# Performance work log

Measured on AMD Instinct MI355X. Metric: run time of the kernel, lower is better.

The kernel has to match this reference:

```python
import jax, jax.numpy as jnp
import numpy as np

H = 4  # num_heads


def _ln(x, g, b, eps=1e-5):
    m = x.mean(-1, keepdims=True)
    v = ((x - m) ** 2).mean(-1, keepdims=True)
    return (x - m) / jnp.sqrt(v + eps) * g + b


def setup_inputs() -> dict:
    key = jax.random.key(0)
    ks = jax.random.split(key, 16)
    B, N, M, dQ, dK, dV = 4, 2048, 2048, 128, 128, 128
    s = 0.02
    return {
        "Q": jax.random.normal(ks[0], (B, N, dQ), jnp.float32),
        "K": jax.random.normal(ks[1], (B, M, dK), jnp.float32),
        "adj_mask": jax.random.randint(ks[2], (B, N, M), 0, 2, jnp.int32),
        "Wq": jax.random.normal(ks[3], (dQ, dV), jnp.float32) * s,
        "bq": jnp.zeros((dV,), jnp.float32),
        "Wk": jax.random.normal(ks[4], (dK, dV), jnp.float32) * s,
        "bk": jnp.zeros((dV,), jnp.float32),
        "Wv": jax.random.normal(ks[5], (dK, dV), jnp.float32) * s,
        "bv": jnp.zeros((dV,), jnp.float32),
        "Wr1": jax.random.normal(ks[6], (dV, dV), jnp.float32) * s,
        "br1": jnp.zeros((dV,), jnp.float32),
        "Wr2": jax.random.normal(ks[7], (dV, dV), jnp.float32) * s,
        "br2": jnp.zeros((dV,), jnp.float32),
        "g0": jnp.ones((dV,), jnp.float32),
        "be0": jnp.zeros((dV,), jnp.float32),
        "g1": jnp.ones((dV,), jnp.float32),
        "be1": jnp.zeros((dV,), jnp.float32),
    }


def reference(Q, K, adj_mask, Wq, bq, Wk, bk, Wv, bv, Wr1, br1, Wr2, br2, g0, be0, g1, be1):
    B, N, _ = Q.shape
    M = K.shape[1]
    dV = Wq.shape[1]
    dh = dV // H
    Qp = Q @ Wq + bq   # [B,N,dV]
    Kp = K @ Wk + bk   # [B,M,dV]
    Vp = K @ Wv + bv   # [B,M,dV]
    # torch: split dim_V into H chunks, cat along dim 0 -> head-major [H*B, L, dh]
    def to_heads(x, L):
        return x.reshape(B, L, H, dh).transpose(2, 0, 1, 3).reshape(H * B, L, dh)
    Qh, Kh, Vh = to_heads(Qp, N), to_heads(Kp, M), to_heads(Vp, M)
    attn = jnp.einsum('bnd,bmd->bnm', Qh, Kh) / jnp.sqrt(jnp.float32(dh))  # [H*B,N,M]
    # torch repeat_interleave(mask, H, dim=0) gives batch-major order -- faithful
    mask = jnp.repeat(adj_mask, H, axis=0)
    attn = jnp.where(mask == 0, -jnp.inf, attn)
    A = jax.nn.softmax(attn, axis=2)
    O = Qh + jnp.einsum('bnm,bmd->bnd', A, Vh)  # [H*B,N,dh]
    # recombine heads back to [B,N,dV] (intended split(dim=0)/cat(dim=2))
    O = O.reshape(H, B, N, dh).transpose(1, 2, 0, 3).reshape(B, N, dV)
    O = _ln(O, g0, be0)
    O = O + (jax.nn.relu(O @ Wr1 + br1) @ Wr2 + br2)
    return _ln(O, g1, be1)
```

## Files before the change

### kernel.cpp

```cpp
#include <hip/hip_runtime.h>
#include <hip/hip_bf16.h>


typedef short bf16x8 __attribute__((ext_vector_type(8)));
typedef float f32x4 __attribute__((ext_vector_type(4)));

#define BN 4
#define SEQ 2048
#define DIM 128
#define NH 4
#define DH 32
#define ROWS (BN * SEQ)
#define MS 4
#define MWORDS (SEQ / 32)

static __device__ __forceinline__ unsigned short f2bf(float f) {
    __hip_bfloat16 h = __float2bfloat16(f);
    return *reinterpret_cast<unsigned short*>(&h);
}
static __device__ __forceinline__ float bf2f(unsigned short u) {
    union { unsigned int i; float f; } cv;
    cv.i = ((unsigned int)u) << 16;
    return cv.f;
}
static __device__ __forceinline__ unsigned int pack2bf(float a, float b) {
    return (unsigned int)f2bf(a) | ((unsigned int)f2bf(b) << 16);
}

__global__ __launch_bounds__(256) void pack_prep(
    const int* __restrict__ adj,
    const float* __restrict__ Wq, const float* __restrict__ Wk,
    const float* __restrict__ Wv, const float* __restrict__ W1,
    const float* __restrict__ W2,
    unsigned int* __restrict__ bits, unsigned short* __restrict__ WT)
{
    const int bx = blockIdx.x;
    const int t = threadIdx.x;
    if (bx >= 1024) {
        const float* Ws[5] = {Wq, Wk, Wv, W1, W2};
        const float* W = Ws[bx - 1024];
        unsigned short* out = WT + (bx - 1024) * DIM * DIM;
        for (int i = t; i < DIM * DIM; i += 256) {
            int n = i >> 7, k = i & 127;
            out[i] = f2bf(W[k * DIM + n]);
        }
        return;
    }
    __shared__ unsigned int sB[8][65];
    const int q0 = bx * 8;
#pragma unroll
    for (int i = 0; i < 2; ++i) {
        int widl = i * 256 + t;
        int ql = widl >> 6, wd = widl & 63;
        const int4* src = (const int4*)(adj + (long)(q0 + ql) * SEQ + wd * 32);
        unsigned int w = 0;
#pragma unroll
        for (int j = 0; j < 8; ++j) {
            int4 v = src[j];
            w |= (((unsigned)v.x & 1u) << (4 * j))
               | (((unsigned)v.y & 1u) << (4 * j + 1))
               | (((unsigned)v.z & 1u) << (4 * j + 2))
               | (((unsigned)v.w & 1u) << (4 * j + 3));
        }
        sB[ql][wd] = w;
    }
    __syncthreads();
    const int h = q0 >> 11, qh0 = q0 & 2047;
#pragma unroll
    for (int i = 0; i < 2; ++i) {
        int idx = i * 256 + t;
        int wd = idx >> 3, ql = idx & 7;
        bits[((long)h * MWORDS + wd) * SEQ + qh0 + ql] = sB[ql][wd];
    }
}

__global__ __launch_bounds__(256) void proj_kernel(
    const float* __restrict__ Q, const float* __restrict__ K,
    const float* __restrict__ bq, const float* __restrict__ bk,
    const float* __restrict__ bv, const unsigned short* __restrict__ WT,
    float* __restrict__ Qp, unsigned short* __restrict__ Qb,
    unsigned short* __restrict__ Kb, unsigned short* __restrict__ Vt)
{
    __shared__ __align__(16) unsigned short sX[32][136];
    __shared__ __align__(16) unsigned short sY[32][137];

    const int proj = blockIdx.y;
    const int rowbase = blockIdx.x * 32;
    const float* X = (proj == 0) ? Q : K;
    const unsigned short* Wt = WT + proj * DIM * DIM;
    const float* bias = (proj == 0) ? bq : (proj == 1) ? bk : bv;
    const int bidx = rowbase >> 11;
    const int srowbase = rowbase & 2047;

    const int t = threadIdx.x;
#pragma unroll
    for (int i = 0; i < 4; ++i) {
        int idx = i * 256 + t;
        int row = idx >> 5, c4 = (idx & 31) * 4;
        float4 v = *(const float4*)(X + (long)(rowbase + row) * DIM + c4);
        sX[row][c4 + 0] = f2bf(v.x);
        sX[row][c4 + 1] = f2bf(v.y);
        sX[row][c4 + 2] = f2bf(v.z);
        sX[row][c4 + 3] = f2bf(v.w);
    }
    __syncthreads();

    const int w = t >> 6, lane = t & 63;
    const int n16 = lane & 15, quad = lane >> 4;

    f32x4 acc[2][2];
#pragma unroll
    for (int r = 0; r < 2; ++r)
#pragma unroll
        for (int ct = 0; ct < 2; ++ct)
            acc[r][ct] = (f32x4){0.f, 0.f, 0.f, 0.f};

    for (int ks = 0; ks < 4; ++ks) {
        bf16x8 bfrag[2];
#pragma unroll
        for (int ct = 0; ct < 2; ++ct) {
            int ncol = w * 32 + ct * 16 + n16;
            bfrag[ct] = *(const bf16x8*)(Wt + ncol * DIM + ks * 32 + quad * 8);
        }
#pragma unroll
        for (int r = 0; r < 2; ++r) {
            bf16x8 afrag = *(const bf16x8*)(&sX[r * 16 + n16][ks * 32 + quad * 8]);
#pragma unroll
            for (int ct = 0; ct < 2; ++ct)
                acc[r][ct] = __builtin_amdgcn_mfma_f32_16x16x32_bf16(
                    afrag, bfrag[ct], acc[r][ct], 0, 0, 0);
        }
    }

#pragma unroll
    for (int r = 0; r < 2; ++r) {
#pragma unroll
        for (int ct = 0; ct < 2; ++ct) {
            int col = w * 32 + ct * 16 + n16;
            int hh = col >> 5, dd = col & 31;
            float bv_ = bias[col];
#pragma unroll
            for (int i = 0; i < 4; ++i) {
                int lrow = r * 16 + quad * 4 + i;
                int grow = rowbase + lrow;
                int srow = srowbase + lrow;
                float val = acc[r][ct][i] + bv_;
                if (proj == 0) {
                    Qp[(long)grow * DIM + col] = val;
                    Qb[((long)(hh * BN + bidx) * SEQ + srow) * DH + dd]
                        = f2bf(val * 0.17677669529663687f);
                } else if (proj == 1) {
                    Kb[((long)(hh * BN + bidx) * SEQ + srow) * DH + dd] = f2bf(val);
                } else {
                    sY[lrow][col] = f2bf(val);
                }
            }
        }
    }
    if (proj == 2) {
        __syncthreads();
#pragma unroll
        for (int i = 0; i < 16; ++i) {
            int idx = i * 256 + t;
            int c = idx >> 5, m = idx & 31;
            Vt[((long)bidx * DIM + c) * SEQ + srowbase + m] = sY[m][c];
        }
    }
}

__global__ __launch_bounds__(256, 2) void attn_kernel(
    const unsigned short* __restrict__ Qb, const unsigned short* __restrict__ Kb,
    const unsigned short* __restrict__ Vt, const unsigned int* __restrict__ mbits,
    unsigned short* __restrict__ Opart, float* __restrict__ Lpart)
{
    __shared__ __align__(16) unsigned short sP[4][32][68];

    const int id = blockIdx.x;
    const int combo = id & 15;
    const int qidx = id >> 4;
    const int h = combo >> 2;
    const int sp = combo & 3;
    const int qbase = qidx * 32;
    const int t = threadIdx.x;
    const int b = t >> 6;
    const int lane = t & 63, n16 = lane & 15, quad = lane >> 4;

    const unsigned short* Qh = Qb + ((long)(h * BN + b) * SEQ) * DH + quad * 8;
    const unsigned short* Kp = Kb + ((long)(h * BN + b) * SEQ) * DH + quad * 8;
    const unsigned short* Vp = Vt + ((long)b * DIM + h * DH) * SEQ + quad * 8;
    const unsigned int*   Mp = mbits + ((long)h * MWORDS + sp * 16) * SEQ + qbase + n16;

    bf16x8 qfrag[2];
#pragma unroll
    for (int r = 0; r < 2; ++r)
        qfrag[r] = *(const bf16x8*)(Qh + (long)(qbase + r * 16 + n16) * DH);

    f32x4 o[2][2];
    float lsum[2];
#pragma unroll
    for (int r = 0; r < 2; ++r) {
#pragma unroll
        for (int ct = 0; ct < 2; ++ct) o[r][ct] = (f32x4){0.f, 0.f, 0.f, 0.f};
        lsum[r] = 0.f;
    }

    bf16x8 kf[2][2];
    unsigned int mw[2][2];
    const int mb0 = sp * 512;

#pragma unroll
    for (int c = 0; c < 2; ++c)
        kf[0][c] = *(const bf16x8*)(Kp + (long)(mb0 + c * 16 + n16) * DH);
#pragma unroll
    for (int r = 0; r < 2; ++r) mw[0][r] = Mp[r * 16];

    const f32x4 zero4 = {0.f, 0.f, 0.f, 0.f};

#pragma unroll
    for (int mt = 0; mt < 16; ++mt) {
        const int cur = mt & 1, nxt = cur ^ 1;
        const int mbc = mb0 + mt * 32;
        bf16x8 vf0 = *(const bf16x8*)(Vp + (long)(0 * 16 + n16) * SEQ + mbc);
        bf16x8 vf1 = *(const bf16x8*)(Vp + (long)(1 * 16 + n16) * SEQ + mbc);
        if (mt < 15) {
            const int mb = mbc + 32;
#pragma unroll
            for (int c = 0; c < 2; ++c)
                kf[nxt][c] = *(const bf16x8*)(Kp + (long)(mb + c * 16 + n16) * DH);
#pragma unroll
            for (int r = 0; r < 2; ++r) mw[nxt][r] = Mp[(long)(mt + 1) * SEQ + r * 16];
        }
#pragma unroll
        for (int r = 0; r < 2; ++r) {
            f32x4 st[2];
#pragma unroll
            for (int c = 0; c < 2; ++c)
                st[c] = __builtin_amdgcn_mfma_f32_16x16x32_bf16(
                    kf[cur][c], qfrag[r], zero4, 0, 0, 0);
            const unsigned int wm = mw[cur][r];
            float p[2][4];
#pragma unroll
            for (int c = 0; c < 2; ++c)
#pragma unroll
                for (int i = 0; i < 4; ++i) {
                    float e = __expf(st[c][i]);
                    p[c][i] = ((wm >> (c * 16 + quad * 4 + i)) & 1u) ? e : 0.f;
                    lsum[r] += p[c][i];
                }
#pragma unroll
            for (int c = 0; c < 2; ++c) {
                uint2 wv;
                wv.x = pack2bf(p[c][0], p[c][1]);
                wv.y = pack2bf(p[c][2], p[c][3]);
                *(uint2*)&sP[b][r * 16 + n16][c * 16 + quad * 4] = wv;
            }
        }
#pragma unroll
        for (int r = 0; r < 2; ++r) {
            bf16x8 pa = *(const bf16x8*)(&sP[b][r * 16 + n16][quad * 8]);
            o[r][0] = __builtin_amdgcn_mfma_f32_16x16x32_bf16(pa, vf0, o[r][0], 0, 0, 0);
            o[r][1] = __builtin_amdgcn_mfma_f32_16x16x32_bf16(pa, vf1, o[r][1], 0, 0, 0);
        }
    }

#pragma unroll
    for (int r = 0; r < 2; ++r) {
        lsum[r] += __shfl_xor(lsum[r], 16, 64);
        lsum[r] += __shfl_xor(lsum[r], 32, 64);
    }

#pragma unroll
    for (int r = 0; r < 2; ++r)
#pragma unroll
        for (int ct = 0; ct < 2; ++ct)
#pragma unroll
            for (int i = 0; i < 4; ++i)
                sP[b][r * 16 + quad * 4 + i][ct * 16 + n16] = f2bf(o[r][ct][i]);
    {
        const uint4 w0 = *(const uint4*)&sP[b][lane >> 1][(lane & 1) * 16];
        const uint4 w1 = *(const uint4*)&sP[b][lane >> 1][(lane & 1) * 16 + 8];
        unsigned short* Ob = Opart
            + ((((long)sp * NH + h) * BN + b) * SEQ + qbase) * 32;
        *(uint4*)(Ob + (long)lane * 16)     = w0;
        *(uint4*)(Ob + (long)lane * 16 + 8) = w1;
    }

    if (quad == 0) {
#pragma unroll
        for (int r = 0; r < 2; ++r)
            Lpart[(((long)sp * BN + b) * NH + h) * SEQ + qbase + r * 16 + n16] = lsum[r];
    }
}

__global__ __launch_bounds__(256) void epi_kernel(
    const float* __restrict__ Qp, const unsigned short* __restrict__ Opart,
    const float* __restrict__ Lpart, const unsigned short* __restrict__ WT,
    const float* __restrict__ br1, const float* __restrict__ br2,
    const float* __restrict__ g0, const float* __restrict__ be0,
    const float* __restrict__ g1, const float* __restrict__ be1,
    float* __restrict__ out)
{
    __shared__ __align__(16) unsigned short sXb[16][136];
    __shared__ __align__(16) unsigned short sHb[16][136];
    __shared__ __align__(16) float sXf[16][132];

    const int rowbase = blockIdx.x * 16;
    const int t = threadIdx.x;
    const int row = t >> 4, col8 = (t & 15) * 8;
    const int grow = rowbase + row;
    const int bidx = grow >> 11;
    const int srow = grow & 2047;
    const int head = col8 >> 5;
    const int dd = col8 & 31;

    {
        float l = 0.f;
#pragma unroll
        for (int s = 0; s < MS; ++s)
            l += Lpart[(((long)s * BN + bidx) * NH + head) * SEQ + srow];
        float linv = 1.f / l;

        float ovf[8];
#pragma unroll
        for (int j = 0; j < 8; ++j) ovf[j] = 0.f;
#pragma unroll
        for (int s = 0; s < MS; ++s) {
            bf16x8 p = *(const bf16x8*)(Opart
                + ((((long)s * NH + head) * BN + bidx) * SEQ + srow) * 32 + dd);
#pragma unroll
            for (int j = 0; j < 8; ++j) ovf[j] += bf2f((unsigned short)p[j]);
        }

        float vals[8];
        float sum = 0.f, ss = 0.f;
#pragma unroll
        for (int j = 0; j < 8; j += 4) {
            float4 qv = *(const float4*)(Qp + (long)grow * DIM + col8 + j);
            vals[j + 0] = qv.x + ovf[j + 0] * linv;
            vals[j + 1] = qv.y + ovf[j + 1] * linv;
            vals[j + 2] = qv.z + ovf[j + 2] * linv;
            vals[j + 3] = qv.w + ovf[j + 3] * linv;
#pragma unroll
            for (int u = 0; u < 4; ++u) { sum += vals[j + u]; ss += vals[j + u] * vals[j + u]; }
        }
        sum += __shfl_xor(sum, 1, 64); sum += __shfl_xor(sum, 2, 64);
        sum += __shfl_xor(sum, 4, 64); sum += __shfl_xor(sum, 8, 64);
        ss  += __shfl_xor(ss, 1, 64);  ss  += __shfl_xor(ss, 2, 64);
        ss  += __shfl_xor(ss, 4, 64);  ss  += __shfl_xor(ss, 8, 64);
        float mean = sum * (1.f / 128.f);
        float var  = ss * (1.f / 128.f) - mean * mean;
        float rstd = rsqrtf(var + 1e-5f);
#pragma unroll
        for (int j = 0; j < 8; ++j) {
            int col = col8 + j;
            float x = (vals[j] - mean) * rstd * g0[col] + be0[col];
            sXf[row][col] = x;
            sXb[row][col] = f2bf(x);
        }
    }
    __syncthreads();

    const int w = t >> 6, lane = t & 63;
    const int n16 = lane & 15, quad = lane >> 4;
    const unsigned short* W1t = WT + 3 * DIM * DIM;
    const unsigned short* W2t = WT + 4 * DIM * DIM;

    f32x4 acc[2];
#pragma unroll
    for (int ct = 0; ct < 2; ++ct) acc[ct] = (f32x4){0.f, 0.f, 0.f, 0.f};
    for (int ks = 0; ks < 4; ++ks) {
        bf16x8 afrag = *(const bf16x8*)(&sXb[n16][ks * 32 + quad * 8]);
#pragma unroll
        for (int ct = 0; ct < 2; ++ct) {
            bf16x8 bfrag = *(const bf16x8*)(W1t + (w * 32 + ct * 16 + n16) * DIM + ks * 32 + quad * 8);
            acc[ct] = __builtin_amdgcn_mfma_f32_16x16x32_bf16(afrag, bfrag, acc[ct], 0, 0, 0);
        }
    }
#pragma unroll
    for (int ct = 0; ct < 2; ++ct) {
        int col = w * 32 + ct * 16 + n16;
        float bb = br1[col];
#pragma unroll
        for (int i = 0; i < 4; ++i) {
            float hv = acc[ct][i] + bb;
            sHb[quad * 4 + i][col] = f2bf(fmaxf(hv, 0.f));
        }
    }
    __syncthreads();

    f32x4 acc2[2];
#pragma unroll
    for (int ct = 0; ct < 2; ++ct) acc2[ct] = (f32x4){0.f, 0.f, 0.f, 0.f};
    for (int ks = 0; ks < 4; ++ks) {
        bf16x8 afrag = *(const bf16x8*)(&sHb[n16][ks * 32 + quad * 8]);
#pragma unroll
        for (int ct = 0; ct < 2; ++ct) {
            bf16x8 bfrag = *(const bf16x8*)(W2t + (w * 32 + ct * 16 + n16) * DIM + ks * 32 + quad * 8);
            acc2[ct] = __builtin_amdgcn_mfma_f32_16x16x32_bf16(afrag, bfrag, acc2[ct], 0, 0, 0);
        }
    }
    float yv[2][4];
#pragma unroll
    for (int ct = 0; ct < 2; ++ct) {
        int col = w * 32 + ct * 16 + n16;
        float bb = br2[col];
#pragma unroll
        for (int i = 0; i < 4; ++i)
            yv[ct][i] = acc2[ct][i] + bb + sXf[quad * 4 + i][col];
    }
    __syncthreads();
#pragma unroll
    for (int ct = 0; ct < 2; ++ct) {
        int col = w * 32 + ct * 16 + n16;
#pragma unroll
        for (int i = 0; i < 4; ++i)
            sXf[quad * 4 + i][col] = yv[ct][i];
    }
    __syncthreads();

    {
        float vals[8];
        float sum = 0.f, ss = 0.f;
#pragma unroll
        for (int j = 0; j < 8; ++j) {
            float v = sXf[row][col8 + j];
            vals[j] = v; sum += v; ss += v * v;
        }
        sum += __shfl_xor(sum, 1, 64); sum += __shfl_xor(sum, 2, 64);
        sum += __shfl_xor(sum, 4, 64); sum += __shfl_xor(sum, 8, 64);
        ss  += __shfl_xor(ss, 1, 64);  ss  += __shfl_xor(ss, 2, 64);
        ss  += __shfl_xor(ss, 4, 64);  ss  += __shfl_xor(ss, 8, 64);
        float mean = sum * (1.f / 128.f);
        float var  = ss * (1.f / 128.f) - mean * mean;
        float rstd = rsqrtf(var + 1e-5f);
        float* op = out + (long)grow * DIM + col8;
#pragma unroll
        for (int j = 0; j < 8; j += 4) {
            float4 ov;
            int col = col8 + j;
            ov.x = (vals[j + 0] - mean) * rstd * g1[col + 0] + be1[col + 0];
            ov.y = (vals[j + 1] - mean) * rstd * g1[col + 1] + be1[col + 1];
            ov.z = (vals[j + 2] - mean) * rstd * g1[col + 2] + be1[col + 2];
            ov.w = (vals[j + 3] - mean) * rstd * g1[col + 3] + be1[col + 3];
            *(float4*)(op + j) = ov;
        }
    }
}

extern "C" void kernel_launch(void* const* d_in, const int* in_sizes, int n_in,
                              void* d_out, int out_size, void* d_ws, size_t ws_size,
                              hipStream_t stream) {
    const float* Q   = (const float*)d_in[0];
    const float* K   = (const float*)d_in[1];
    const int*   adj = (const int*)d_in[2];
    const float* Wq  = (const float*)d_in[3];
    const float* bq  = (const float*)d_in[4];
    const float* Wk  = (const float*)d_in[5];
    const float* bk  = (const float*)d_in[6];
    const float* Wv  = (const float*)d_in[7];
    const float* bv  = (const float*)d_in[8];
    const float* Wr1 = (const float*)d_in[9];
    const float* br1 = (const float*)d_in[10];
    const float* Wr2 = (const float*)d_in[11];
    const float* br2 = (const float*)d_in[12];
    const float* g0  = (const float*)d_in[13];
    const float* be0 = (const float*)d_in[14];
    const float* g1  = (const float*)d_in[15];
    const float* be1 = (const float*)d_in[16];
    float* out = (float*)d_out;

    float* Qp             = (float*)d_ws;
    unsigned short* Opart = (unsigned short*)(Qp + (long)ROWS * DIM);
    float* Lpart          = (float*)(Opart + (long)MS * ROWS * DIM);
    unsigned short* Qb    = (unsigned short*)(Lpart + (long)MS * BN * NH * SEQ);
    unsigned short* Kb    = Qb + (long)ROWS * DIM;
    unsigned short* Vt    = Kb + (long)ROWS * DIM;
    unsigned short* WT    = Vt + (long)ROWS * DIM;
    unsigned int*   bits  = (unsigned int*)(WT + 5 * DIM * DIM);

    pack_prep<<<1029, 256, 0, stream>>>(adj, Wq, Wk, Wv, Wr1, Wr2, bits, WT);
    proj_kernel<<<dim3(256, 3), 256, 0, stream>>>(Q, K, bq, bk, bv, WT,
                                                  Qp, Qb, Kb, Vt);
    attn_kernel<<<1024, 256, 0, stream>>>(Qb, Kb, Vt, bits, Opart, Lpart);
    epi_kernel<<<512, 256, 0, stream>>>(Qp, Opart, Lpart, WT, br1, br2,
                                        g0, be0, g1, be1, out);
}
```

Measured before the change: 181.5 us.

## Fuse mask packing, weight transpose and QKV projection into one prep kernel

Merges the mask bit-packing/weight-transpose kernel and the projection kernel into a single launch. Projection blocks now convert and transpose their own Wq/Wk/Wv into shared memory instead of reading a pre-transposed global copy, which removes the dependency between the two kernels and one launch. The cost is that each of the 768 projection blocks redoes a full 128x128 weight transpose, and the shared memory per block grows to about 52KB, which may reduce occupancy.

Result: no change. 178.8 us (-1.5%).

```diff
diff --git a/kernel.cpp b/kernel.cpp
--- a/kernel.cpp
+++ b/kernel.cpp
@@ -27,72 +27,83 @@
     return (unsigned int)f2bf(a) | ((unsigned int)f2bf(b) << 16);
 }
 
-__global__ __launch_bounds__(256) void pack_prep(
-    const int* __restrict__ adj,
+__global__ __launch_bounds__(256) void fused_prep(
+    const float* __restrict__ Q, const float* __restrict__ K,
+    const float* __restrict__ bq, const float* __restrict__ bk,
+    const float* __restrict__ bv,
     const float* __restrict__ Wq, const float* __restrict__ Wk,
     const float* __restrict__ Wv, const float* __restrict__ W1,
-    const float* __restrict__ W2,
+    const float* __restrict__ W2, const int* __restrict__ adj,
+    float* __restrict__ Qp, unsigned short* __restrict__ Qb,
+    unsigned short* __restrict__ Kb, unsigned short* __restrict__ Vt,
     unsigned int* __restrict__ bits, unsigned short* __restrict__ WT)
 {
+    __shared__ __align__(16) unsigned char smem[52288];
     const int bx = blockIdx.x;
     const int t = threadIdx.x;
-    if (bx >= 1024) {
-        const float* Ws[5] = {Wq, Wk, Wv, W1, W2};
-        const float* W = Ws[bx - 1024];
-        unsigned short* out = WT + (bx - 1024) * DIM * DIM;
+
+    if (bx >= 1792) {
+        const float* W = (bx == 1792) ? W1 : W2;
+        unsigned short* out = WT + (bx - 1792) * DIM * DIM;
         for (int i = t; i < DIM * DIM; i += 256) {
             int n = i >> 7, k = i & 127;
             out[i] = f2bf(W[k * DIM + n]);
         }
         return;
     }
-    __shared__ unsigned int sB[8][65];
-    const int q0 = bx * 8;
-#pragma unroll
-    for (int i = 0; i < 2; ++i) {
-        int widl = i * 256 + t;
-        int ql = widl >> 6, wd = widl & 63;
-        const int4* src = (const int4*)(adj + (long)(q0 + ql) * SEQ + wd * 32);
-        unsigned int w = 0;
-#pragma unroll
-        for (int j = 0; j < 8; ++j) {
-            int4 v = src[j];
-            w |= (((unsigned)v.x & 1u) << (4 * j))
-               | (((unsigned)v.y & 1u) << (4 * j + 1))
-               | (((unsigned)v.z & 1u) << (4 * j + 2))
-               | (((unsigned)v.w & 1u) << (4 * j + 3));
-        }
-        sB[ql][wd] = w;
-    }
-    __syncthreads();
-    const int h = q0 >> 11, qh0 = q0 & 2047;
-#pragma unroll
-    for (int i = 0; i < 2; ++i) {
-        int idx = i * 256 + t;
-        int wd = idx >> 3, ql = idx & 7;
-        bits[((long)h * MWORDS + wd) * SEQ + qh0 + ql] = sB[ql][wd];
-    }
-}
-
-__global__ __launch_bounds__(256) void proj_kernel(
-    const float* __restrict__ Q, const float* __restrict__ K,
-    const float* __restrict__ bq, const float* __restrict__ bk,
-    const float* __restrict__ bv, const unsigned short* __restrict__ WT,
-    float* __restrict__ Qp, unsigned short* __restrict__ Qb,
-    unsigned short* __restrict__ Kb, unsigned short* __restrict__ Vt)
-{
-    __shared__ __align__(16) unsigned short sX[32][136];
-    __shared__ __align__(16) unsigned short sY[32][137];
-
-    const int proj = blockIdx.y;
-    const int rowbase = blockIdx.x * 32;
+
+    if (bx >= 768) {
+        unsigned int (*sB)[65] = (unsigned int(*)[65])smem;
+        const int q0 = (bx - 768) * 8;
+#pragma unroll
+        for (int i = 0; i < 2; ++i) {
+            int widl = i * 256 + t;
+            int ql = widl >> 6, wd = widl & 63;
+            const int4* src = (const int4*)(adj + (long)(q0 + ql) * SEQ + wd * 32);
+            unsigned int w = 0;
+#pragma unroll
+            for (int j = 0; j < 8; ++j) {
+                int4 v = src[j];
+                w |= (((unsigned)v.x & 1u) << (4 * j))
+                   | (((unsigned)v.y & 1u) << (4 * j + 1))
+                   | (((unsigned)v.z & 1u) << (4 * j + 2))
+                   | (((unsigned)v.w & 1u) << (4 * j + 3));
+            }
+            sB[ql][wd] = w;
+        }
+        __syncthreads();
+        const int h = q0 >> 11, qh0 = q0 & 2047;
+#pragma unroll
+        for (int i = 0; i < 2; ++i) {
+            int idx = i * 256 + t;
+            int wd = idx >> 3, ql = idx & 7;
+            bits[((long)h * MWORDS + wd) * SEQ + qh0 + ql] = sB[ql][wd];
+        }
+        return;
+    }
+
+    unsigned short (*sW)[136] = (unsigned short(*)[136])smem;
+    unsigned short (*sX)[136] = (unsigned short(*)[136])(smem + 34816);
+    unsigned short (*sY)[137] = (unsigned short(*)[137])(smem + 43520);
+
+    const int proj = bx >> 8;
+    const int rowbase = (bx & 255) * 32;
     const float* X = (proj == 0) ? Q : K;
-    const unsigned short* Wt = WT + proj * DIM * DIM;
+    const float* W = (proj == 0) ? Wq : (proj == 1) ? Wk : Wv;
     const float* bias = (proj == 0) ? bq : (proj == 1) ? bk : bv;
     const int bidx = rowbase >> 11;
     const int srowbase = rowbase & 2047;
 
-    const int t = threadIdx.x;
+#pragma unroll
+    for (int i = 0; i < 16; ++i) {
+        int idx = i * 256 + t;
+        int k = idx >> 5, n4 = (idx & 31) * 4;
+        float4 v = *(const float4*)(W + k * DIM + n4);
+        sW[n4 + 0][k] = f2bf(v.x);
+        sW[n4 + 1][k] = f2bf(v.y);
+        sW[n4 + 2][k] = f2bf(v.z);
+        sW[n4 + 3][k] = f2bf(v.w);
+    }
 #pragma unroll
     for (int i = 0; i < 4; ++i) {
         int idx = i * 256 + t;
@@ -120,7 +131,7 @@
 #pragma unroll
         for (int ct = 0; ct < 2; ++ct) {
             int ncol = w * 32 + ct * 16 + n16;
-            bfrag[ct] = *(const bf16x8*)(Wt + ncol * DIM + ks * 32 + quad * 8);
+            bfrag[ct] = *(const bf16x8*)(&sW[ncol][ks * 32 + quad * 8]);
         }
 #pragma unroll
         for (int r = 0; r < 2; ++r) {
@@ -362,8 +373,8 @@
 
     const int w = t >> 6, lane = t & 63;
     const int n16 = lane & 15, quad = lane >> 4;
-    const unsigned short* W1t = WT + 3 * DIM * DIM;
-    const unsigned short* W2t = WT + 4 * DIM * DIM;
+    const unsigned short* W1t = WT;
+    const unsigned short* W2t = WT + DIM * DIM;
 
     f32x4 acc[2];
 #pragma unroll
@@ -476,11 +487,10 @@
     unsigned short* Kb    = Qb + (long)ROWS * DIM;
     unsigned short* Vt    = Kb + (long)ROWS * DIM;
     unsigned short* WT    = Vt + (long)ROWS * DIM;
-    unsigned int*   bits  = (unsigned int*)(WT + 5 * DIM * DIM);
-
-    pack_prep<<<1029, 256, 0, stream>>>(adj, Wq, Wk, Wv, Wr1, Wr2, bits, WT);
-    proj_kernel<<<dim3(256, 3), 256, 0, stream>>>(Q, K, bq, bk, bv, WT,
-                                                  Qp, Qb, Kb, Vt);
+    unsigned int*   bits  = (unsigned int*)(WT + 2 * DIM * DIM);
+
+    fused_prep<<<1794, 256, 0, stream>>>(Q, K, bq, bk, bv, Wq, Wk, Wv, Wr1, Wr2,
+                                         adj, Qp, Qb, Kb, Vt, bits, WT);
     attn_kernel<<<1024, 256, 0, stream>>>(Qb, Kb, Vt, bits, Opart, Lpart);
     epi_kernel<<<512, 256, 0, stream>>>(Qp, Opart, Lpart, WT, br1, br2,
                                         g0, be0, g1, be1, out);
```
